# Kernel optimization log

Measured on AMD Instinct MI355X. Metric: run time of the kernel, lower is better.

The kernel has to match this reference:

```python
import jax, jax.numpy as jnp
import numpy as np

QUERY_DIM = 512
KV_DIM = 64
N_AUX = 8
B = 65536
EPS = 1e-5


def setup_inputs() -> dict:
    key = jax.random.key(0)
    k1, k2, k3, k4, k5 = jax.random.split(key, 5)
    query = jax.random.normal(k1, (B, QUERY_DIM), dtype=jnp.float32)
    kv_stack = jax.random.normal(k2, (B, N_AUX, KV_DIM), dtype=jnp.float32)
    # Linear weights (torch nn.Linear stores W as [out, in]; y = x @ W.T)
    w_q = jax.random.normal(k3, (KV_DIM, QUERY_DIM), dtype=jnp.float32) / np.sqrt(QUERY_DIM)
    w_k = jax.random.normal(k4, (KV_DIM, KV_DIM), dtype=jnp.float32) / np.sqrt(KV_DIM)
    w_v = jax.random.normal(k5, (KV_DIM, KV_DIM), dtype=jnp.float32) / np.sqrt(KV_DIM)
    ln_gamma = jnp.ones((KV_DIM,), dtype=jnp.float32)
    ln_beta = jnp.zeros((KV_DIM,), dtype=jnp.float32)
    return {"query": query, "kv_stack": kv_stack, "w_q": w_q, "w_k": w_k,
            "w_v": w_v, "ln_gamma": ln_gamma, "ln_beta": ln_beta}


def reference(query, kv_stack, w_q, w_k, w_v, ln_gamma, ln_beta):
    scale = KV_DIM ** (-0.5)
    q = query @ w_q.T                                  # (B, kv_dim)
    k = jnp.einsum('bnd,ed->bne', kv_stack, w_k)       # (B, n_aux, kv_dim)
    v = jnp.einsum('bnd,ed->bne', kv_stack, w_v)       # (B, n_aux, kv_dim)
    scores = jnp.einsum('bd,bnd->bn', q, k) * scale    # (B, n_aux)
    attn_w = jax.nn.softmax(scores, axis=-1)
    out = jnp.einsum('bn,bnd->bd', attn_w, v)          # (B, kv_dim)
    # LayerNorm over last dim
    mu = jnp.mean(out, axis=-1, keepdims=True)
    var = jnp.var(out, axis=-1, keepdims=True)
    normed = (out - mu) / jnp.sqrt(var + EPS)
    return normed * ln_gamma + ln_beta
```

## Files before the change

kernel.cpp:

```cpp
#include <hip/hip_runtime.h>

#define QD 512
#define KD 64
#define NR 32
#define LDA 136
#define LDT 68
#define LDU 72

typedef __attribute__((ext_vector_type(8))) short short8;
typedef __attribute__((ext_vector_type(4))) float f32x4;
typedef __attribute__((ext_vector_type(4))) unsigned short u16x4;

static __device__ __forceinline__ unsigned short f2bf(float f) {
  unsigned u = __builtin_bit_cast(unsigned, f);
  u += 0x7FFFu + ((u >> 16) & 1u);
  return (unsigned short)(u >> 16);
}
static __device__ __forceinline__ float bf2f(unsigned short s) {
  return __builtin_bit_cast(float, (unsigned)s << 16);
}
static __device__ __forceinline__ short8 pack8(f32x4 a, f32x4 b) {
  short8 r;
  r[0] = (short)f2bf(a[0]); r[1] = (short)f2bf(a[1]);
  r[2] = (short)f2bf(a[2]); r[3] = (short)f2bf(a[3]);
  r[4] = (short)f2bf(b[0]); r[5] = (short)f2bf(b[1]);
  r[6] = (short)f2bf(b[2]); r[7] = (short)f2bf(b[3]);
  return r;
}

__global__ __launch_bounds__(256) void prep_kernel(
    const float* __restrict__ w_q, const float* __restrict__ w_k,
    const float* __restrict__ w_v, unsigned short* __restrict__ mt,
    unsigned short* __restrict__ wvb) {
  const int tid = (int)(blockIdx.x * 256 + threadIdx.x);
  if (tid < QD * KD) {
    const int c = tid >> 9;
    const int d = tid & 511;
    float acc = 0.f;
#pragma unroll 8
    for (int e = 0; e < 64; ++e)
      acc = fmaf(w_q[e * QD + d], w_k[e * KD + c], acc);
    mt[c * QD + d] = f2bf(acc);
  } else {
    const int i = tid - QD * KD;
    if (i < KD * KD) wvb[i] = f2bf(w_v[i]);
  }
}

__global__ __launch_bounds__(256) void fused_kernel(
    const float* __restrict__ query,
    const float* __restrict__ kv,
    const unsigned short* __restrict__ mt,
    const unsigned short* __restrict__ wvb,
    const float* __restrict__ gamma,
    const float* __restrict__ beta,
    float* __restrict__ out) {
  __shared__ char shbuf[NR * LDA * 2];
  unsigned short* lds_A = (unsigned short*)shbuf;
  float* lds_t = (float*)shbuf;
  __shared__ unsigned short lds_u[NR * LDU];

  const int tid  = (int)threadIdx.x;
  const int w    = tid >> 6;
  const int l    = tid & 63;
  const int m    = l & 15;
  const int quad = l >> 4;
  const long b0  = (long)blockIdx.x * NR;

  const unsigned short* mrow = mt + (w * 16 + m) * QD + quad * 8;
  short8 bf_cur[4], bf_nxt[4];
#pragma unroll
  for (int ks = 0; ks < 4; ++ks)
    bf_cur[ks] = *(const short8*)(mrow + ks * 32);

  f32x4 acc[2];
  acc[0] = (f32x4){0.f, 0.f, 0.f, 0.f};
  acc[1] = (f32x4){0.f, 0.f, 0.f, 0.f};

  const int srow = tid >> 3;
  const int cseg = tid & 7;
  const float* qbase = query + (b0 + srow) * QD + cseg * 16;
  unsigned short* abase = lds_A + srow * LDA + cseg * 16;

  f32x4 stg[4];
#pragma unroll
  for (int i = 0; i < 4; ++i) stg[i] = *(const f32x4*)(qbase + i * 4);

#pragma unroll
  for (int kc = 0; kc < 4; ++kc) {
#pragma unroll
    for (int i = 0; i < 4; ++i)
      *(u16x4*)(abase + i * 4) = (u16x4){f2bf(stg[i][0]), f2bf(stg[i][1]),
                                         f2bf(stg[i][2]), f2bf(stg[i][3])};
    __syncthreads();
    if (kc < 3) {
      const float* nq = qbase + (kc + 1) * 128;
#pragma unroll
      for (int i = 0; i < 4; ++i) stg[i] = *(const f32x4*)(nq + i * 4);
      const unsigned short* mn = mrow + (kc + 1) * 128;
#pragma unroll
      for (int ks = 0; ks < 4; ++ks)
        bf_nxt[ks] = *(const short8*)(mn + ks * 32);
    }
#pragma unroll
    for (int ks2 = 0; ks2 < 4; ++ks2) {
#pragma unroll
      for (int rt = 0; rt < 2; ++rt) {
        short8 af = *(const short8*)(lds_A + (rt * 16 + m) * LDA + ks2 * 32 + quad * 8);
        acc[rt] = __builtin_amdgcn_mfma_f32_16x16x32_bf16(af, bf_cur[ks2],
                                                          acc[rt], 0, 0, 0);
      }
    }
    __syncthreads();
    if (kc < 3) {
#pragma unroll
      for (int ks = 0; ks < 4; ++ks) bf_cur[ks] = bf_nxt[ks];
    }
  }

#pragma unroll
  for (int rt = 0; rt < 2; ++rt)
#pragma unroll
    for (int r2 = 0; r2 < 4; ++r2)
      lds_t[(rt * 16 + quad * 4 + r2) * LDT + w * 16 + m] = acc[rt][r2];
  __syncthreads();

  const int rl = w * 8 + (l >> 3);
  const int o8 = l & 7;
  const int db = o8 * 8;
  const long brow = b0 + rl;

  const float* tp = lds_t + rl * LDT + db;
  f32x4 tv0 = ((const f32x4*)tp)[0];
  f32x4 tv1 = ((const f32x4*)tp)[1];

  float s[8];
  short8 kvb[8];
#pragma unroll
  for (int n = 0; n < 8; ++n) {
    const float* kp = kv + (brow * 8 + n) * 64 + db;
    f32x4 k0 = ((const f32x4*)kp)[0];
    f32x4 k1 = ((const f32x4*)kp)[1];
    f32x4 d = tv0 * k0 + tv1 * k1;
    s[n] = d[0] + d[1] + d[2] + d[3];
    kvb[n] = pack8(k0, k1);
  }
#pragma unroll
  for (int n = 0; n < 8; ++n) {
    s[n] += __shfl_xor(s[n], 1, 64);
    s[n] += __shfl_xor(s[n], 2, 64);
    s[n] += __shfl_xor(s[n], 4, 64);
  }
  float mx = s[0];
#pragma unroll
  for (int n = 1; n < 8; ++n) mx = fmaxf(mx, s[n]);
  float ev[8];
  float esum = 0.f;
#pragma unroll
  for (int n = 0; n < 8; ++n) { ev[n] = __expf((s[n] - mx) * 0.125f); esum += ev[n]; }
  const float rinv = 1.0f / esum;

  f32x4 u0 = {0.f, 0.f, 0.f, 0.f}, u1 = u0;
#pragma unroll
  for (int n = 0; n < 8; ++n) {
    const float a = ev[n];
    short8 p = kvb[n];
    u0 += a * (f32x4){bf2f((unsigned short)p[0]), bf2f((unsigned short)p[1]),
                      bf2f((unsigned short)p[2]), bf2f((unsigned short)p[3])};
    u1 += a * (f32x4){bf2f((unsigned short)p[4]), bf2f((unsigned short)p[5]),
                      bf2f((unsigned short)p[6]), bf2f((unsigned short)p[7])};
  }
  u0 *= rinv; u1 *= rinv;
  *(short8*)(lds_u + rl * LDU + db) = pack8(u0, u1);
  __syncthreads();

  short8 wvf0 = *(const short8*)(wvb + (w * 16 + m) * 64 + quad * 8);
  short8 wvf1 = *(const short8*)(wvb + (w * 16 + m) * 64 + 32 + quad * 8);
  f32x4 o[2];
  o[0] = (f32x4){0.f, 0.f, 0.f, 0.f};
  o[1] = (f32x4){0.f, 0.f, 0.f, 0.f};
#pragma unroll
  for (int rt = 0; rt < 2; ++rt) {
    short8 a0 = *(const short8*)(lds_u + (rt * 16 + m) * LDU + quad * 8);
    o[rt] = __builtin_amdgcn_mfma_f32_16x16x32_bf16(a0, wvf0, o[rt], 0, 0, 0);
    short8 a1 = *(const short8*)(lds_u + (rt * 16 + m) * LDU + 32 + quad * 8);
    o[rt] = __builtin_amdgcn_mfma_f32_16x16x32_bf16(a1, wvf1, o[rt], 0, 0, 0);
  }
#pragma unroll
  for (int rt = 0; rt < 2; ++rt)
#pragma unroll
    for (int r2 = 0; r2 < 4; ++r2)
      lds_t[(rt * 16 + quad * 4 + r2) * LDT + w * 16 + m] = o[rt][r2];
  __syncthreads();

  const float* op = lds_t + rl * LDT + db;
  f32x4 x0 = ((const f32x4*)op)[0];
  f32x4 x1 = ((const f32x4*)op)[1];
  f32x4 sv = x0 + x1;
  f32x4 sq = x0 * x0 + x1 * x1;
  float s1 = sv[0] + sv[1] + sv[2] + sv[3];
  float s2 = sq[0] + sq[1] + sq[2] + sq[3];
  s1 += __shfl_xor(s1, 1, 64); s1 += __shfl_xor(s1, 2, 64); s1 += __shfl_xor(s1, 4, 64);
  s2 += __shfl_xor(s2, 1, 64); s2 += __shfl_xor(s2, 2, 64); s2 += __shfl_xor(s2, 4, 64);
  const float mu   = s1 * 0.015625f;
  const float var  = s2 * 0.015625f - mu * mu;
  const float rstd = rsqrtf(var + 1e-5f);
  const float* gp = gamma + db;
  const float* bp = beta + db;
  float* dst = out + brow * 64 + db;
  {
    f32x4 g0 = ((const f32x4*)gp)[0], g1 = ((const f32x4*)gp)[1];
    f32x4 e0 = ((const f32x4*)bp)[0], e1 = ((const f32x4*)bp)[1];
    ((f32x4*)dst)[0] = (x0 - mu) * rstd * g0 + e0;
    ((f32x4*)dst)[1] = (x1 - mu) * rstd * g1 + e1;
  }
}

extern "C" void kernel_launch(void* const* d_in, const int* in_sizes, int n_in,
                              void* d_out, int out_size, void* d_ws, size_t ws_size,
                              hipStream_t stream) {
  const float* query = (const float*)d_in[0];
  const float* kv    = (const float*)d_in[1];
  const float* w_q   = (const float*)d_in[2];
  const float* w_k   = (const float*)d_in[3];
  const float* w_v   = (const float*)d_in[4];
  const float* gamma = (const float*)d_in[5];
  const float* beta  = (const float*)d_in[6];
  float* out = (float*)d_out;

  unsigned short* mt  = (unsigned short*)d_ws;
  unsigned short* wvb = mt + QD * KD;

  const int Bn = in_sizes[0] / QD;

  prep_kernel<<<(QD * KD + KD * KD + 255) / 256, 256, 0, stream>>>(w_q, w_k, w_v, mt, wvb);
  fused_kernel<<<Bn / NR, 256, 0, stream>>>(query, kv, mt, wvb, gamma, beta, out);
}
```

Baseline: 291.2 us.

## Make each wave own 16 rows independently, loading query fragments directly into registers

Restructures the fused kernel so each wavefront processes its own 16 batch rows end-to-end across all 64 output columns. Query fragments are loaded straight from global memory into MFMA operand registers, with no LDS staging and no block-wide barriers; wave-local LDS scratch and lgkmcnt waits replace __syncthreads. The goal is to remove barrier stalls and the LDS round trip for the query tile, which leaves the kernel closer to bandwidth-bound on the query and kv reads. In exchange, each wave now loads the full mt matrix (more L2 traffic per row) and uses more accumulator registers. Each lane's query loads are 32-byte strided chunks and may coalesce less well.

```diff
diff --git a/kernel.cpp b/kernel.cpp
--- a/kernel.cpp
+++ b/kernel.cpp
@@ -2,14 +2,11 @@
 
 #define QD 512
 #define KD 64
-#define NR 32
-#define LDA 136
 #define LDT 68
 #define LDU 72
 
 typedef __attribute__((ext_vector_type(8))) short short8;
 typedef __attribute__((ext_vector_type(4))) float f32x4;
-typedef __attribute__((ext_vector_type(4))) unsigned short u16x4;
 
 static __device__ __forceinline__ unsigned short f2bf(float f) {
   unsigned u = __builtin_bit_cast(unsigned, f);
@@ -27,6 +24,8 @@
   r[6] = (short)f2bf(b[2]); r[7] = (short)f2bf(b[3]);
   return r;
 }
+
+#define WAVE_LDS_FENCE() asm volatile("s_waitcnt lgkmcnt(0)" ::: "memory")
 
 __global__ __launch_bounds__(256) void prep_kernel(
     const float* __restrict__ w_q, const float* __restrict__ w_k,
@@ -55,162 +54,159 @@
     const float* __restrict__ gamma,
     const float* __restrict__ beta,
     float* __restrict__ out) {
-  __shared__ char shbuf[NR * LDA * 2];
-  unsigned short* lds_A = (unsigned short*)shbuf;
-  float* lds_t = (float*)shbuf;
-  __shared__ unsigned short lds_u[NR * LDU];
+  __shared__ __align__(16) float lds_t_all[4][16 * LDT];
+  __shared__ __align__(16) unsigned short lds_u_all[4][16 * LDU];
 
   const int tid  = (int)threadIdx.x;
   const int w    = tid >> 6;
   const int l    = tid & 63;
   const int m    = l & 15;
   const int quad = l >> 4;
-  const long b0  = (long)blockIdx.x * NR;
-
-  const unsigned short* mrow = mt + (w * 16 + m) * QD + quad * 8;
-  short8 bf_cur[4], bf_nxt[4];
-#pragma unroll
-  for (int ks = 0; ks < 4; ++ks)
-    bf_cur[ks] = *(const short8*)(mrow + ks * 32);
-
-  f32x4 acc[2];
-  acc[0] = (f32x4){0.f, 0.f, 0.f, 0.f};
-  acc[1] = (f32x4){0.f, 0.f, 0.f, 0.f};
-
-  const int srow = tid >> 3;
-  const int cseg = tid & 7;
-  const float* qbase = query + (b0 + srow) * QD + cseg * 16;
-  unsigned short* abase = lds_A + srow * LDA + cseg * 16;
-
-  f32x4 stg[4];
-#pragma unroll
-  for (int i = 0; i < 4; ++i) stg[i] = *(const f32x4*)(qbase + i * 4);
-
-#pragma unroll
-  for (int kc = 0; kc < 4; ++kc) {
-#pragma unroll
-    for (int i = 0; i < 4; ++i)
-      *(u16x4*)(abase + i * 4) = (u16x4){f2bf(stg[i][0]), f2bf(stg[i][1]),
-                                         f2bf(stg[i][2]), f2bf(stg[i][3])};
-    __syncthreads();
-    if (kc < 3) {
-      const float* nq = qbase + (kc + 1) * 128;
-#pragma unroll
-      for (int i = 0; i < 4; ++i) stg[i] = *(const f32x4*)(nq + i * 4);
-      const unsigned short* mn = mrow + (kc + 1) * 128;
-#pragma unroll
-      for (int ks = 0; ks < 4; ++ks)
-        bf_nxt[ks] = *(const short8*)(mn + ks * 32);
-    }
-#pragma unroll
-    for (int ks2 = 0; ks2 < 4; ++ks2) {
-#pragma unroll
-      for (int rt = 0; rt < 2; ++rt) {
-        short8 af = *(const short8*)(lds_A + (rt * 16 + m) * LDA + ks2 * 32 + quad * 8);
-        acc[rt] = __builtin_amdgcn_mfma_f32_16x16x32_bf16(af, bf_cur[ks2],
-                                                          acc[rt], 0, 0, 0);
-      }
-    }
-    __syncthreads();
-    if (kc < 3) {
-#pragma unroll
-      for (int ks = 0; ks < 4; ++ks) bf_cur[ks] = bf_nxt[ks];
-    }
-  }
-
-#pragma unroll
-  for (int rt = 0; rt < 2; ++rt)
-#pragma unroll
-    for (int r2 = 0; r2 < 4; ++r2)
-      lds_t[(rt * 16 + quad * 4 + r2) * LDT + w * 16 + m] = acc[rt][r2];
-  __syncthreads();
-
-  const int rl = w * 8 + (l >> 3);
-  const int o8 = l & 7;
-  const int db = o8 * 8;
-  const long brow = b0 + rl;
-
-  const float* tp = lds_t + rl * LDT + db;
-  f32x4 tv0 = ((const f32x4*)tp)[0];
-  f32x4 tv1 = ((const f32x4*)tp)[1];
-
-  float s[8];
-  short8 kvb[8];
-#pragma unroll
-  for (int n = 0; n < 8; ++n) {
-    const float* kp = kv + (brow * 8 + n) * 64 + db;
-    f32x4 k0 = ((const f32x4*)kp)[0];
-    f32x4 k1 = ((const f32x4*)kp)[1];
-    f32x4 d = tv0 * k0 + tv1 * k1;
-    s[n] = d[0] + d[1] + d[2] + d[3];
-    kvb[n] = pack8(k0, k1);
-  }
-#pragma unroll
-  for (int n = 0; n < 8; ++n) {
-    s[n] += __shfl_xor(s[n], 1, 64);
-    s[n] += __shfl_xor(s[n], 2, 64);
-    s[n] += __shfl_xor(s[n], 4, 64);
-  }
-  float mx = s[0];
-#pragma unroll
-  for (int n = 1; n < 8; ++n) mx = fmaxf(mx, s[n]);
-  float ev[8];
-  float esum = 0.f;
-#pragma unroll
-  for (int n = 0; n < 8; ++n) { ev[n] = __expf((s[n] - mx) * 0.125f); esum += ev[n]; }
-  const float rinv = 1.0f / esum;
-
-  f32x4 u0 = {0.f, 0.f, 0.f, 0.f}, u1 = u0;
-#pragma unroll
-  for (int n = 0; n < 8; ++n) {
-    const float a = ev[n];
-    short8 p = kvb[n];
-    u0 += a * (f32x4){bf2f((unsigned short)p[0]), bf2f((unsigned short)p[1]),
-                      bf2f((unsigned short)p[2]), bf2f((unsigned short)p[3])};
-    u1 += a * (f32x4){bf2f((unsigned short)p[4]), bf2f((unsigned short)p[5]),
-                      bf2f((unsigned short)p[6]), bf2f((unsigned short)p[7])};
-  }
-  u0 *= rinv; u1 *= rinv;
-  *(short8*)(lds_u + rl * LDU + db) = pack8(u0, u1);
-  __syncthreads();
-
-  short8 wvf0 = *(const short8*)(wvb + (w * 16 + m) * 64 + quad * 8);
-  short8 wvf1 = *(const short8*)(wvb + (w * 16 + m) * 64 + 32 + quad * 8);
-  f32x4 o[2];
-  o[0] = (f32x4){0.f, 0.f, 0.f, 0.f};
-  o[1] = (f32x4){0.f, 0.f, 0.f, 0.f};
-#pragma unroll
-  for (int rt = 0; rt < 2; ++rt) {
-    short8 a0 = *(const short8*)(lds_u + (rt * 16 + m) * LDU + quad * 8);
-    o[rt] = __builtin_amdgcn_mfma_f32_16x16x32_bf16(a0, wvf0, o[rt], 0, 0, 0);
-    short8 a1 = *(const short8*)(lds_u + (rt * 16 + m) * LDU + 32 + quad * 8);
-    o[rt] = __builtin_amdgcn_mfma_f32_16x16x32_bf16(a1, wvf1, o[rt], 0, 0, 0);
-  }
-#pragma unroll
-  for (int rt = 0; rt < 2; ++rt)
-#pragma unroll
-    for (int r2 = 0; r2 < 4; ++r2)
-      lds_t[(rt * 16 + quad * 4 + r2) * LDT + w * 16 + m] = o[rt][r2];
-  __syncthreads();
-
-  const float* op = lds_t + rl * LDT + db;
-  f32x4 x0 = ((const f32x4*)op)[0];
-  f32x4 x1 = ((const f32x4*)op)[1];
-  f32x4 sv = x0 + x1;
-  f32x4 sq = x0 * x0 + x1 * x1;
-  float s1 = sv[0] + sv[1] + sv[2] + sv[3];
-  float s2 = sq[0] + sq[1] + sq[2] + sq[3];
-  s1 += __shfl_xor(s1, 1, 64); s1 += __shfl_xor(s1, 2, 64); s1 += __shfl_xor(s1, 4, 64);
-  s2 += __shfl_xor(s2, 1, 64); s2 += __shfl_xor(s2, 2, 64); s2 += __shfl_xor(s2, 4, 64);
-  const float mu   = s1 * 0.015625f;
-  const float var  = s2 * 0.015625f - mu * mu;
-  const float rstd = rsqrtf(var + 1e-5f);
-  const float* gp = gamma + db;
-  const float* bp = beta + db;
-  float* dst = out + brow * 64 + db;
-  {
-    f32x4 g0 = ((const f32x4*)gp)[0], g1 = ((const f32x4*)gp)[1];
-    f32x4 e0 = ((const f32x4*)bp)[0], e1 = ((const f32x4*)bp)[1];
+
+  float* lds_t = lds_t_all[w];
+  unsigned short* lds_u = lds_u_all[w];
+
+  const long row0 = ((long)blockIdx.x * 4 + w) * 16;
+
+  const float* qbase = query + (row0 + m) * QD + quad * 8;
+  const unsigned short* mbase = mt + m * QD + quad * 8;
+
+  f32x4 acc[4];
+#pragma unroll
+  for (int ct = 0; ct < 4; ++ct) acc[ct] = (f32x4){0.f, 0.f, 0.f, 0.f};
+
+  f32x4 q0 = ((const f32x4*)qbase)[0];
+  f32x4 q1 = ((const f32x4*)qbase)[1];
+  f32x4 p0 = ((const f32x4*)(qbase + 32))[0];
+  f32x4 p1 = ((const f32x4*)(qbase + 32))[1];
+  short8 bc[4], bn[4];
+#pragma unroll
+  for (int ct = 0; ct < 4; ++ct)
+    bc[ct] = *(const short8*)(mbase + ct * 16 * QD);
+
+#pragma unroll
+  for (int ks = 0; ks < 16; ++ks) {
+    short8 af = pack8(q0, q1);
+    if (ks < 15) {
+#pragma unroll
+      for (int ct = 0; ct < 4; ++ct)
+        bn[ct] = *(const short8*)(mbase + ct * 16 * QD + (ks + 1) * 32);
+    }
+    q0 = p0; q1 = p1;
+    if (ks < 14) {
+      const float* np = qbase + (ks + 2) * 32;
+      p0 = ((const f32x4*)np)[0];
+      p1 = ((const f32x4*)np)[1];
+    }
+#pragma unroll
+    for (int ct = 0; ct < 4; ++ct)
+      acc[ct] = __builtin_amdgcn_mfma_f32_16x16x32_bf16(af, bc[ct], acc[ct], 0, 0, 0);
+#pragma unroll
+    for (int ct = 0; ct < 4; ++ct) bc[ct] = bn[ct];
+  }
+
+#pragma unroll
+  for (int ct = 0; ct < 4; ++ct)
+#pragma unroll
+    for (int r = 0; r < 4; ++r)
+      lds_t[(quad * 4 + r) * LDT + ct * 16 + m] = acc[ct][r];
+  WAVE_LDS_FENCE();
+
+  const int rseg = l >> 3;
+  const int o8   = l & 7;
+  const int db   = o8 * 8;
+
+  f32x4 g0 = ((const f32x4*)(gamma + db))[0];
+  f32x4 g1 = ((const f32x4*)(gamma + db))[1];
+  f32x4 e0 = ((const f32x4*)(beta + db))[0];
+  f32x4 e1 = ((const f32x4*)(beta + db))[1];
+
+#pragma unroll
+  for (int p = 0; p < 2; ++p) {
+    const int rl = p * 8 + rseg;
+    const long brow = row0 + rl;
+    const float* tp = lds_t + rl * LDT + db;
+    f32x4 tv0 = ((const f32x4*)tp)[0];
+    f32x4 tv1 = ((const f32x4*)tp)[1];
+
+    float s[8];
+    short8 kvb[8];
+#pragma unroll
+    for (int n = 0; n < 8; ++n) {
+      const float* kp = kv + (brow * 8 + n) * 64 + db;
+      f32x4 k0 = ((const f32x4*)kp)[0];
+      f32x4 k1 = ((const f32x4*)kp)[1];
+      f32x4 d = tv0 * k0 + tv1 * k1;
+      s[n] = d[0] + d[1] + d[2] + d[3];
+      kvb[n] = pack8(k0, k1);
+    }
+#pragma unroll
+    for (int n = 0; n < 8; ++n) {
+      s[n] += __shfl_xor(s[n], 1, 64);
+      s[n] += __shfl_xor(s[n], 2, 64);
+      s[n] += __shfl_xor(s[n], 4, 64);
+    }
+    float mx = s[0];
+#pragma unroll
+    for (int n = 1; n < 8; ++n) mx = fmaxf(mx, s[n]);
+    float ev[8];
+    float esum = 0.f;
+#pragma unroll
+    for (int n = 0; n < 8; ++n) { ev[n] = __expf((s[n] - mx) * 0.125f); esum += ev[n]; }
+    const float rinv = 1.0f / esum;
+
+    f32x4 u0 = {0.f, 0.f, 0.f, 0.f}, u1 = u0;
+#pragma unroll
+    for (int n = 0; n < 8; ++n) {
+      const float a = ev[n];
+      short8 pk = kvb[n];
+      u0 += a * (f32x4){bf2f((unsigned short)pk[0]), bf2f((unsigned short)pk[1]),
+                        bf2f((unsigned short)pk[2]), bf2f((unsigned short)pk[3])};
+      u1 += a * (f32x4){bf2f((unsigned short)pk[4]), bf2f((unsigned short)pk[5]),
+                        bf2f((unsigned short)pk[6]), bf2f((unsigned short)pk[7])};
+    }
+    u0 *= rinv; u1 *= rinv;
+    *(short8*)(lds_u + rl * LDU + db) = pack8(u0, u1);
+  }
+  WAVE_LDS_FENCE();
+
+  f32x4 o4[4];
+#pragma unroll
+  for (int ct = 0; ct < 4; ++ct) o4[ct] = (f32x4){0.f, 0.f, 0.f, 0.f};
+#pragma unroll
+  for (int ks = 0; ks < 2; ++ks) {
+    short8 ua = *(const short8*)(lds_u + m * LDU + ks * 32 + quad * 8);
+#pragma unroll
+    for (int ct = 0; ct < 4; ++ct) {
+      short8 wf = *(const short8*)(wvb + (ct * 16 + m) * 64 + ks * 32 + quad * 8);
+      o4[ct] = __builtin_amdgcn_mfma_f32_16x16x32_bf16(ua, wf, o4[ct], 0, 0, 0);
+    }
+  }
+
+#pragma unroll
+  for (int ct = 0; ct < 4; ++ct)
+#pragma unroll
+    for (int r = 0; r < 4; ++r)
+      lds_t[(quad * 4 + r) * LDT + ct * 16 + m] = o4[ct][r];
+  WAVE_LDS_FENCE();
+
+#pragma unroll
+  for (int p = 0; p < 2; ++p) {
+    const int rl = p * 8 + rseg;
+    const long brow = row0 + rl;
+    const float* op = lds_t + rl * LDT + db;
+    f32x4 x0 = ((const f32x4*)op)[0];
+    f32x4 x1 = ((const f32x4*)op)[1];
+    f32x4 sv = x0 + x1;
+    f32x4 sq = x0 * x0 + x1 * x1;
+    float s1 = sv[0] + sv[1] + sv[2] + sv[3];
+    float s2 = sq[0] + sq[1] + sq[2] + sq[3];
+    s1 += __shfl_xor(s1, 1, 64); s1 += __shfl_xor(s1, 2, 64); s1 += __shfl_xor(s1, 4, 64);
+    s2 += __shfl_xor(s2, 1, 64); s2 += __shfl_xor(s2, 2, 64); s2 += __shfl_xor(s2, 4, 64);
+    const float mu   = s1 * 0.015625f;
+    const float var  = s2 * 0.015625f - mu * mu;
+    const float rstd = rsqrtf(var + 1e-5f);
+    float* dst = out + brow * 64 + db;
     ((f32x4*)dst)[0] = (x0 - mu) * rstd * g0 + e0;
     ((f32x4*)dst)[1] = (x1 - mu) * rstd * g1 + e1;
   }
@@ -234,5 +230,5 @@
   const int Bn = in_sizes[0] / QD;
 
   prep_kernel<<<(QD * KD + KD * KD + 255) / 256, 256, 0, stream>>>(w_q, w_k, w_v, mt, wvb);
-  fused_kernel<<<Bn / NR, 256, 0, stream>>>(query, kv, mt, wvb, gamma, beta, out);
-}
+  fused_kernel<<<Bn / 64, 256, 0, stream>>>(query, kv, mt, wvb, gamma, beta, out);
+}
```

Result: slower. 303.2 us (+4.1%).

## Stream query and weight tiles into LDS via async global_load_lds double buffering

Applied to the files above, without the earlier changes.

Replaces the register-staged query load and per-wave register prefetch of the projection weights with direct global-to-LDS DMA (global_load_lds, 16 bytes per lane). The K loop is split into 16 chunks of 32 with two ping-pong LDS buffers, and an XOR swizzle is applied on the writes and reads to avoid bank conflicts. Query data now sits in LDS as fp32 and is converted to bf16 right before each MFMA. The aim is to overlap global loads with compute and cut VGPR pressure, at the cost of more barriers per tile, extra conversions, and hand-written vmcnt waits that must track the in-flight DMAs exactly.

```diff
diff --git a/kernel.cpp b/kernel.cpp
--- a/kernel.cpp
+++ b/kernel.cpp
@@ -3,13 +3,11 @@
 #define QD 512
 #define KD 64
 #define NR 32
-#define LDA 136
 #define LDT 68
 #define LDU 72
 
 typedef __attribute__((ext_vector_type(8))) short short8;
 typedef __attribute__((ext_vector_type(4))) float f32x4;
-typedef __attribute__((ext_vector_type(4))) unsigned short u16x4;
 
 static __device__ __forceinline__ unsigned short f2bf(float f) {
   unsigned u = __builtin_bit_cast(unsigned, f);
@@ -26,6 +24,12 @@
   r[4] = (short)f2bf(b[0]); r[5] = (short)f2bf(b[1]);
   r[6] = (short)f2bf(b[2]); r[7] = (short)f2bf(b[3]);
   return r;
+}
+
+static __device__ __forceinline__ void dma16(const void* g, void* l) {
+  __builtin_amdgcn_global_load_lds(
+      (const __attribute__((address_space(1))) void*)g,
+      (__attribute__((address_space(3))) void*)l, 16, 0, 0);
 }
 
 __global__ __launch_bounds__(256) void prep_kernel(
@@ -55,66 +59,56 @@
     const float* __restrict__ gamma,
     const float* __restrict__ beta,
     float* __restrict__ out) {
-  __shared__ char shbuf[NR * LDA * 2];
-  unsigned short* lds_A = (unsigned short*)shbuf;
-  float* lds_t = (float*)shbuf;
-  __shared__ unsigned short lds_u[NR * LDU];
+  __shared__ __align__(16) char regionA[NR * LDT * 4];
+  __shared__ __align__(16) char regionB[8192];
+  float* lds_t = (float*)regionA;
+  unsigned short* lds_u = (unsigned short*)regionB;
 
   const int tid  = (int)threadIdx.x;
   const int w    = tid >> 6;
   const int l    = tid & 63;
   const int m    = l & 15;
   const int quad = l >> 4;
-  const long b0  = (long)blockIdx.x * NR;
-
-  const unsigned short* mrow = mt + (w * 16 + m) * QD + quad * 8;
-  short8 bf_cur[4], bf_nxt[4];
-#pragma unroll
-  for (int ks = 0; ks < 4; ++ks)
-    bf_cur[ks] = *(const short8*)(mrow + ks * 32);
+  const long row0 = (long)blockIdx.x * NR;
+
+  const float* qsrc = query + (row0 + w * 8 + (l >> 3)) * QD
+                            + (((l & 7) ^ ((l >> 3) & 7)) * 4);
+  const unsigned short* msrc = mt + (w * 16 + (l >> 2)) * QD
+                                  + (((l & 3) ^ ((l >> 4) & 3)) * 8);
+  char* qdst = regionA + w * 1024;
+  char* mdst = regionB + w * 1024;
+
+  dma16(qsrc, qdst);            dma16(msrc, mdst);
+  dma16(qsrc + 32, qdst + 4096); dma16(msrc + 32, mdst + 4096);
+
+  const int a0off = m * 128 + (((2 * quad)     ^ (m & 7)) * 16);
+  const int a1off = m * 128 + (((2 * quad + 1) ^ (m & 7)) * 16);
+  const int boff  = (w * 16 + m) * 64 + ((quad ^ (m >> 2)) * 16);
 
   f32x4 acc[2];
   acc[0] = (f32x4){0.f, 0.f, 0.f, 0.f};
   acc[1] = (f32x4){0.f, 0.f, 0.f, 0.f};
 
-  const int srow = tid >> 3;
-  const int cseg = tid & 7;
-  const float* qbase = query + (b0 + srow) * QD + cseg * 16;
-  unsigned short* abase = lds_A + srow * LDA + cseg * 16;
-
-  f32x4 stg[4];
-#pragma unroll
-  for (int i = 0; i < 4; ++i) stg[i] = *(const f32x4*)(qbase + i * 4);
-
-#pragma unroll
-  for (int kc = 0; kc < 4; ++kc) {
-#pragma unroll
-    for (int i = 0; i < 4; ++i)
-      *(u16x4*)(abase + i * 4) = (u16x4){f2bf(stg[i][0]), f2bf(stg[i][1]),
-                                         f2bf(stg[i][2]), f2bf(stg[i][3])};
+#pragma unroll
+  for (int c = 0; c < 16; ++c) {
+    if (c < 15) { asm volatile("s_waitcnt vmcnt(2)" ::: "memory"); }
+    else        { asm volatile("s_waitcnt vmcnt(0)" ::: "memory"); }
     __syncthreads();
-    if (kc < 3) {
-      const float* nq = qbase + (kc + 1) * 128;
-#pragma unroll
-      for (int i = 0; i < 4; ++i) stg[i] = *(const f32x4*)(nq + i * 4);
-      const unsigned short* mn = mrow + (kc + 1) * 128;
-#pragma unroll
-      for (int ks = 0; ks < 4; ++ks)
-        bf_nxt[ks] = *(const short8*)(mn + ks * 32);
-    }
-#pragma unroll
-    for (int ks2 = 0; ks2 < 4; ++ks2) {
-#pragma unroll
-      for (int rt = 0; rt < 2; ++rt) {
-        short8 af = *(const short8*)(lds_A + (rt * 16 + m) * LDA + ks2 * 32 + quad * 8);
-        acc[rt] = __builtin_amdgcn_mfma_f32_16x16x32_bf16(af, bf_cur[ks2],
-                                                          acc[rt], 0, 0, 0);
-      }
+
+    const char* qb = regionA + (c & 1) * 4096;
+    const char* bbuf = regionB + (c & 1) * 4096;
+    short8 bf = *(const short8*)(bbuf + boff);
+#pragma unroll
+    for (int rt = 0; rt < 2; ++rt) {
+      f32x4 g0 = *(const f32x4*)(qb + rt * 2048 + a0off);
+      f32x4 g1 = *(const f32x4*)(qb + rt * 2048 + a1off);
+      short8 af = pack8(g0, g1);
+      acc[rt] = __builtin_amdgcn_mfma_f32_16x16x32_bf16(af, bf, acc[rt], 0, 0, 0);
     }
     __syncthreads();
-    if (kc < 3) {
-#pragma unroll
-      for (int ks = 0; ks < 4; ++ks) bf_cur[ks] = bf_nxt[ks];
+    if (c + 2 < 16) {
+      dma16(qsrc + (c + 2) * 32, qdst + (c & 1) * 4096);
+      dma16(msrc + (c + 2) * 32, mdst + (c & 1) * 4096);
     }
   }
 
@@ -128,7 +122,7 @@
   const int rl = w * 8 + (l >> 3);
   const int o8 = l & 7;
   const int db = o8 * 8;
-  const long brow = b0 + rl;
+  const long brow = row0 + rl;
 
   const float* tp = lds_t + rl * LDT + db;
   f32x4 tv0 = ((const f32x4*)tp)[0];
```

Measured after the change: 293.4 us. Within noise of the previous version (+0.7%).
